# Kernel optimization log

Hardware: AMD Instinct MI355X
Metric: run time of the kernel (lower is better)

The kernel has to match this reference:

```python
import jax, jax.numpy as jnp
import numpy as np

N_NODES = 100000
N_EDGES = 1600000
HIDDEN_DIM = 64
EIGS_DIM = 32


def setup_inputs() -> dict:
    key = jax.random.key(0)
    k1, k2, k3, k4, k5 = jax.random.split(key, 5)
    q = jax.random.normal(k1, (N_NODES, HIDDEN_DIM), dtype=jnp.float32)
    k = jax.random.normal(k2, (N_NODES, HIDDEN_DIM), dtype=jnp.float32)
    v = jax.random.normal(k3, (N_NODES, HIDDEN_DIM), dtype=jnp.float32)
    eigs = jax.random.normal(k4, (N_NODES, EIGS_DIM), dtype=jnp.float32)
    lambda0 = jnp.zeros((1,), dtype=jnp.float32)  # nn.Parameter(torch.zeros(1))
    indices = jax.random.randint(k5, (2, N_EDGES), 0, N_NODES, dtype=jnp.int64)
    return {"q": q, "k": k, "v": v, "eigs": eigs, "lambda0": lambda0,
            "indices": indices}


def reference(q, k, v, eigs, lambda0, indices):
    n = q.shape[0]
    inv_sqrt_dim = 1.0 / jnp.sqrt(jnp.asarray(q.shape[1], dtype=q.dtype))
    i0 = indices[0]  # destination/row node per edge
    i1 = indices[1]  # source/col node per edge

    # per-edge attention logits: gather-dot-product
    x = jnp.sum(q[i0] * k[i1], axis=-1) * inv_sqrt_dim          # [E]
    y = jnp.sum(eigs[i0] * eigs[i1], axis=-1)                   # [E]
    s = x + jnp.exp(lambda0[0]) * y                             # [E]

    # sparse softmax: clamp(exp(s), -5, 5) then segment-normalize by row sum
    e = jnp.clip(jnp.exp(s), -5.0, 5.0)                         # [E]
    denom = jax.ops.segment_sum(e, i0, num_segments=n)          # [N]
    denom = jnp.where(denom == 0.0, 1.0, denom)
    w = e / denom[i0]                                           # [E]

    # spmm: out[r] = sum_{edges with row r} w_e * v[col_e]
    out = jax.ops.segment_sum(w[:, None] * v[i1], i0, num_segments=n)  # [N, D]
    return out
```

## Files before the change

kernel.cpp:

```cpp
#include <hip/hip_runtime.h>


#define HD 64
#define ED 32
#define CAP 64
#define RPP 256
#define PSHIFT 8
#define D1 36
#define NB1 256
#define PCAP 5120
#define SPILL_CAP 131072

__global__ void p1_bin_kernel(const int* __restrict__ idx, int n_edges,
                              int NP, int chunk,
                              int* __restrict__ part, int* __restrict__ gcur,
                              long long* __restrict__ spill,
                              int* __restrict__ spill_cnt,
                              int* __restrict__ flag) {
    extern __shared__ int sm[];
    int* cnt  = sm;
    int* bins = sm + NP;
    int tid = threadIdx.x;

    for (int i = tid; i < NP; i += 256) cnt[i] = 0;
    __syncthreads();

    int e0 = blockIdx.x * chunk;
    int n  = n_edges - e0; if (n > chunk) n = chunk; if (n < 0) n = 0;

    for (int i = tid; i < n; i += 256) {
        int e = e0 + i;
        int r = idx[e];
        int c = idx[n_edges + e];
        int p = r >> PSHIFT;
        int w = ((r & (RPP - 1)) << 17) | c;
        int pos = atomicAdd(&cnt[p], 1);
        if (pos < D1) {
            bins[p * D1 + pos] = w;
        } else {
            int s = atomicAdd(spill_cnt, 1);
            if (s < SPILL_CAP) spill[s] = ((long long)r << 32) | (unsigned)c;
            else *flag = 1;
        }
    }
    __syncthreads();

    for (int p = tid; p < NP; p += 256) {
        int m = cnt[p]; if (m > D1) m = D1;
        if (m > 0) {
            int base = atomicAdd(&gcur[p], m);
            for (int j = 0; j < m; ++j) {
                int slot = base + j;
                int w = bins[p * D1 + j];
                if (slot < PCAP) {
                    part[p * PCAP + slot] = w;
                } else {
                    int r = (p << PSHIFT) | (w >> 17);
                    int c = w & 0x1FFFF;
                    int s = atomicAdd(spill_cnt, 1);
                    if (s < SPILL_CAP) spill[s] = ((long long)r << 32) | (unsigned)c;
                    else *flag = 1;
                }
            }
        }
    }
}

__global__ void p2_bucket_kernel(const int* __restrict__ part,
                                 const int* __restrict__ gcur,
                                 int* __restrict__ count,
                                 int* __restrict__ bucket, int n_nodes) {
    __shared__ int cnt[RPP / 2];
    __shared__ int win[(RPP / 2) * CAP];
    int tid = threadIdx.x;
    if (tid < RPP / 2) cnt[tid] = 0;
    __syncthreads();

    int p    = blockIdx.x >> 1;
    int half = blockIdx.x & 1;
    int n = gcur[p]; if (n > PCAP) n = PCAP;

    for (int i = tid; i < n; i += 256) {
        int w  = part[p * PCAP + i];
        int rl = w >> 17;
        if ((rl >> 7) != half) continue;
        int rh = rl & 127;
        int c  = w & 0x1FFFF;
        int pos = atomicAdd(&cnt[rh], 1);
        if (pos < CAP) win[(rh << 6) + pos] = c;
    }
    __syncthreads();

    int r0 = (p << PSHIFT) + (half << 7);
    int rows = n_nodes - r0;
    if (rows > RPP / 2) rows = RPP / 2;
    if (rows > 0) {
        int nint4 = rows * (CAP / 4);
        int4* dst = (int4*)(bucket + (long long)r0 * CAP);
        const int4* src = (const int4*)win;
        for (int i = tid; i < nint4; i += 256) dst[i] = src[i];
        if (tid < rows) count[r0 + tid] = cnt[tid];
    }
}

__global__ void spill_drain_kernel(const long long* __restrict__ spill,
                                   const int* __restrict__ spill_cnt,
                                   int* __restrict__ count,
                                   int* __restrict__ bucket) {
    int ns = *spill_cnt; if (ns > SPILL_CAP) ns = SPILL_CAP;
    int stride = gridDim.x * blockDim.x;
    for (int t = blockIdx.x * blockDim.x + threadIdx.x; t < ns; t += stride) {
        long long wc = spill[t];
        int r = (int)(wc >> 32);
        int c = (int)(wc & 0xFFFFFFFFLL);
        int pos = atomicAdd(&count[r], 1);
        if (pos < CAP) bucket[(long long)r * CAP + pos] = c;
    }
}

__global__ void repair_zero_kernel(const int* __restrict__ flag,
                                   int* __restrict__ count, int n_nodes) {
    if (*flag == 0) return;
    int t = blockIdx.x * blockDim.x + threadIdx.x;
    if (t < n_nodes) count[t] = 0;
}

__global__ void repair_scatter_kernel(const int* __restrict__ flag,
                                      const int* __restrict__ idx,
                                      int* __restrict__ count,
                                      int* __restrict__ bucket, int n_edges) {
    if (*flag == 0) return;
    int t = blockIdx.x * blockDim.x + threadIdx.x;
    if (t < n_edges) {
        int r = idx[t];
        int c = idx[n_edges + t];
        int p = atomicAdd(&count[r], 1);
        if (p < CAP) bucket[(long long)r * CAP + p] = c;
    }
}

__global__ void bucket_scatter_kernel(const int* __restrict__ idx,
                                      int* __restrict__ count,
                                      int* __restrict__ bucket, int n_edges) {
    int t = blockIdx.x * blockDim.x + threadIdx.x;
    if (t < n_edges) {
        int r = idx[t];
        int c = idx[n_edges + t];
        int p = atomicAdd(&count[r], 1);
        if (p < CAP) bucket[(long long)r * CAP + p] = c;
    }
}

__global__ void row_kernel(const float* __restrict__ q, const float* __restrict__ k,
                           const float* __restrict__ v, const float* __restrict__ eigs,
                           const float* __restrict__ lambda0,
                           const int* __restrict__ counts,
                           const int* __restrict__ col,
                           const int* __restrict__ idx, int n_edges,
                           float* __restrict__ out, int n_nodes) {
    long long tid = (long long)blockIdx.x * blockDim.x + threadIdx.x;
    int r = (int)(tid >> 6);
    if (r >= n_nodes) return;
    int lane = threadIdx.x & 63;
    int sub = lane & 15;
    int grp = lane >> 4;

    int deg = counts[r];
    const float expL = __expf(lambda0[0]);

    if (deg > CAP) {
        float qs = q[(long long)r * HD + lane] * 0.125f;
        float gs = (lane < ED) ? eigs[(long long)r * ED + lane] * expL : 0.f;
        float accs = 0.f, den = 0.f;
        for (int base = 0; base < n_edges; base += 64) {
            int e = base + lane;
            int rr = (e < n_edges) ? idx[e] : -1;
            int cc = (e < n_edges) ? idx[n_edges + e] : 0;
            unsigned long long mm = __ballot(rr == r);
            while (mm) {
                int b = __ffsll(mm) - 1;
                mm &= mm - 1;
                int c = __shfl(cc, b, 64);
                float kb = k[(long long)c * HD + lane];
                float gb = (lane < ED) ? eigs[(long long)c * ED + lane] : 0.f;
                float s = qs * kb + gs * gb;
                #pragma unroll
                for (int off = 32; off > 0; off >>= 1) s += __shfl_xor(s, off, 64);
                float e1 = fminf(__expf(s), 5.0f);
                den += e1;
                accs += e1 * v[(long long)c * HD + lane];
            }
        }
        float inv = (den == 0.f) ? 1.f : __frcp_rn(den);
        out[(long long)r * HD + lane] = accs * inv;
        return;
    }

    long long start = (long long)r * CAP;

    float4 qa = *(const float4*)(q    + (long long)r * HD + sub * 4);
    float2 ga = *(const float2*)(eigs + (long long)r * ED + sub * 2);
    qa.x *= 0.125f; qa.y *= 0.125f; qa.z *= 0.125f; qa.w *= 0.125f;
    ga.x *= expL;   ga.y *= expL;

    float4 acc = make_float4(0.f, 0.f, 0.f, 0.f);
    float den = 0.f;

    for (int base = 0; base < deg; base += 64) {
        int m = deg - base; if (m > 64) m = 64;
        int cl = (lane < m) ? col[start + base + lane] : 0;
        for (int j = 0; j < m; j += 16) {
            int c1 = __shfl(cl, j + grp,      64);
            int c2 = __shfl(cl, j + 4 + grp,  64);
            int c3 = __shfl(cl, j + 8 + grp,  64);
            int c4 = __shfl(cl, j + 12 + grp, 64);
            float4 kb1 = *(const float4*)(k    + (long long)c1 * HD + sub * 4);
            float2 gb1 = *(const float2*)(eigs + (long long)c1 * ED + sub * 2);
            float4 vv1 = *(const float4*)(v    + (long long)c1 * HD + sub * 4);
            float4 kb2 = *(const float4*)(k    + (long long)c2 * HD + sub * 4);
            float2 gb2 = *(const float2*)(eigs + (long long)c2 * ED + sub * 2);
            float4 vv2 = *(const float4*)(v    + (long long)c2 * HD + sub * 4);
            float4 kb3 = *(const float4*)(k    + (long long)c3 * HD + sub * 4);
            float2 gb3 = *(const float2*)(eigs + (long long)c3 * ED + sub * 2);
            float4 vv3 = *(const float4*)(v    + (long long)c3 * HD + sub * 4);
            float4 kb4 = *(const float4*)(k    + (long long)c4 * HD + sub * 4);
            float2 gb4 = *(const float2*)(eigs + (long long)c4 * ED + sub * 2);
            float4 vv4 = *(const float4*)(v    + (long long)c4 * HD + sub * 4);

            float s1 = qa.x*kb1.x + qa.y*kb1.y + qa.z*kb1.z + qa.w*kb1.w
                     + ga.x*gb1.x + ga.y*gb1.y;
            float s2 = qa.x*kb2.x + qa.y*kb2.y + qa.z*kb2.z + qa.w*kb2.w
                     + ga.x*gb2.x + ga.y*gb2.y;
            float s3 = qa.x*kb3.x + qa.y*kb3.y + qa.z*kb3.z + qa.w*kb3.w
                     + ga.x*gb3.x + ga.y*gb3.y;
            float s4 = qa.x*kb4.x + qa.y*kb4.y + qa.z*kb4.z + qa.w*kb4.w
                     + ga.x*gb4.x + ga.y*gb4.y;
            #pragma unroll
            for (int off = 8; off > 0; off >>= 1) {
                s1 += __shfl_xor(s1, off, 64);
                s2 += __shfl_xor(s2, off, 64);
                s3 += __shfl_xor(s3, off, 64);
                s4 += __shfl_xor(s4, off, 64);
            }
            float e1 = fminf(__expf(s1), 5.0f);
            float e2 = fminf(__expf(s2), 5.0f);
            float e3 = fminf(__expf(s3), 5.0f);
            float e4 = fminf(__expf(s4), 5.0f);

            if (j + grp < m) {
                den += e1;
                acc.x += e1 * vv1.x; acc.y += e1 * vv1.y;
                acc.z += e1 * vv1.z; acc.w += e1 * vv1.w;
            }
            if (j + 4 + grp < m) {
                den += e2;
                acc.x += e2 * vv2.x; acc.y += e2 * vv2.y;
                acc.z += e2 * vv2.z; acc.w += e2 * vv2.w;
            }
            if (j + 8 + grp < m) {
                den += e3;
                acc.x += e3 * vv3.x; acc.y += e3 * vv3.y;
                acc.z += e3 * vv3.z; acc.w += e3 * vv3.w;
            }
            if (j + 12 + grp < m) {
                den += e4;
                acc.x += e4 * vv4.x; acc.y += e4 * vv4.y;
                acc.z += e4 * vv4.z; acc.w += e4 * vv4.w;
            }
        }
    }

    #pragma unroll
    for (int off = 16; off < 64; off <<= 1) {
        acc.x += __shfl_xor(acc.x, off, 64);
        acc.y += __shfl_xor(acc.y, off, 64);
        acc.z += __shfl_xor(acc.z, off, 64);
        acc.w += __shfl_xor(acc.w, off, 64);
        den   += __shfl_xor(den,   off, 64);
    }

    if (grp == 0) {
        float inv = (den == 0.0f) ? 1.0f : __frcp_rn(den);
        float4 o = make_float4(acc.x * inv, acc.y * inv, acc.z * inv, acc.w * inv);
        *(float4*)(out + (long long)r * HD + sub * 4) = o;
    }
}

__global__ void edge_fused_kernel(const float* __restrict__ q,
                                  const float* __restrict__ k,
                                  const float* __restrict__ v,
                                  const float* __restrict__ eigs,
                                  const float* __restrict__ lambda0,
                                  const int* __restrict__ idx,
                                  float* __restrict__ denom,
                                  float* __restrict__ out, int n_edges) {
    long long gid = (long long)blockIdx.x * blockDim.x + threadIdx.x;
    int lane = threadIdx.x & 63;
    int edge = (int)(gid >> 4);
    int sub  = (int)(gid & 15);
    int valid = (edge < n_edges);
    int ec = valid ? edge : (n_edges - 1);
    int i0 = idx[ec];
    int i1 = idx[n_edges + ec];
    const float expL = __expf(lambda0[0]);
    float4 qa = *(const float4*)(q + (long long)i0 * HD + sub * 4);
    float4 kb = *(const float4*)(k + (long long)i1 * HD + sub * 4);
    float c = (qa.x*kb.x + qa.y*kb.y + qa.z*kb.z + qa.w*kb.w) * 0.125f;
    float2 ea = *(const float2*)(eigs + (long long)i0 * ED + sub * 2);
    float2 eb = *(const float2*)(eigs + (long long)i1 * ED + sub * 2);
    c += expL * (ea.x * eb.x + ea.y * eb.y);
    #pragma unroll
    for (int off = 8; off > 0; off >>= 1) c += __shfl_xor(c, off, 64);
    float e = fminf(__expf(c), 5.0f);
    if (valid && sub == 0) atomicAdd(&denom[i0], e);
    #pragma unroll
    for (int j = 0; j < 4; ++j) {
        float ej = __shfl(e,     j * 16, 64);
        int   r  = __shfl(i0,    j * 16, 64);
        int   s  = __shfl(i1,    j * 16, 64);
        int   vj = __shfl(valid, j * 16, 64);
        if (vj) {
            float vv = v[(long long)s * HD + lane];
            atomicAdd(&out[(long long)r * HD + lane], ej * vv);
        }
    }
}

__global__ void normalize_kernel(float* __restrict__ out,
                                 const float* __restrict__ denom, int n_nodes) {
    int t = blockIdx.x * blockDim.x + threadIdx.x;
    int total = n_nodes * (HD / 4);
    if (t >= total) return;
    int row = t >> 4;
    float d = denom[row];
    float inv = (d == 0.0f) ? 1.0f : __frcp_rn(d);
    float4* o4 = (float4*)out;
    float4 x = o4[t];
    x.x *= inv; x.y *= inv; x.z *= inv; x.w *= inv;
    o4[t] = x;
}

extern "C" void kernel_launch(void* const* d_in, const int* in_sizes, int n_in,
                              void* d_out, int out_size, void* d_ws, size_t ws_size,
                              hipStream_t stream) {
    const float* q       = (const float*)d_in[0];
    const float* k       = (const float*)d_in[1];
    const float* v       = (const float*)d_in[2];
    const float* eigs    = (const float*)d_in[3];
    const float* lambda0 = (const float*)d_in[4];
    const int*   idx     = (const int*)d_in[5];

    const int n_edges = in_sizes[5] / 2;
    const int n_nodes = in_sizes[0] / HD;

    const int NP = (n_nodes + RPP - 1) / RPP;
    const int eb = (n_edges + 255) / 256;
    long long rthreads = (long long)n_nodes * 64;
    const int rb = (int)((rthreads + 255) / 256);

    size_t need1 = ((size_t)n_nodes + (size_t)n_nodes * CAP
                    + (size_t)NP * PCAP + NP + 2) * sizeof(int)
                 + (size_t)SPILL_CAP * sizeof(long long);
    size_t need2 = ((size_t)n_nodes + (size_t)n_nodes * CAP) * sizeof(int);

    if (ws_size >= need1) {
        int* count     = (int*)d_ws;
        int* bucket    = count + n_nodes;
        int* part      = bucket + (size_t)n_nodes * CAP;
        int* gcur      = part + (size_t)NP * PCAP;
        int* spill_cnt = gcur + NP;
        int* flag      = spill_cnt + 1;
        long long* spill = (long long*)(flag + 1);

        hipMemsetAsync(gcur, 0, (size_t)(NP + 2) * sizeof(int), stream);

        int chunk = (n_edges + NB1 - 1) / NB1;
        size_t smbytes = (size_t)NP * (1 + D1) * sizeof(int);
        p1_bin_kernel<<<NB1, 256, smbytes, stream>>>(idx, n_edges, NP, chunk,
                                                     part, gcur, spill,
                                                     spill_cnt, flag);
        p2_bucket_kernel<<<2 * NP, 256, 0, stream>>>(part, gcur, count, bucket,
                                                     n_nodes);
        spill_drain_kernel<<<256, 256, 0, stream>>>(spill, spill_cnt, count,
                                                    bucket);
        repair_zero_kernel<<<(n_nodes + 255) / 256, 256, 0, stream>>>(flag, count,
                                                                      n_nodes);
        repair_scatter_kernel<<<eb, 256, 0, stream>>>(flag, idx, count, bucket,
                                                      n_edges);
        row_kernel<<<rb, 256, 0, stream>>>(q, k, v, eigs, lambda0, count, bucket,
                                           idx, n_edges, (float*)d_out, n_nodes);
    } else if (ws_size >= need2) {
        int* count  = (int*)d_ws;
        int* bucket = count + n_nodes;
        hipMemsetAsync(count, 0, (size_t)n_nodes * sizeof(int), stream);
        bucket_scatter_kernel<<<eb, 256, 0, stream>>>(idx, count, bucket, n_edges);
        row_kernel<<<rb, 256, 0, stream>>>(q, k, v, eigs, lambda0, count, bucket,
                                           idx, n_edges, (float*)d_out, n_nodes);
    } else {
        float* denom = (float*)d_ws;
        hipMemsetAsync(denom, 0, (size_t)n_nodes * sizeof(float), stream);
        hipMemsetAsync(d_out, 0, (size_t)out_size * sizeof(float), stream);
        long long threads = (long long)n_edges * 16;
        int grid = (int)((threads + 255) / 256);
        edge_fused_kernel<<<grid, 256, 0, stream>>>(q, k, v, eigs, lambda0, idx,
                                                    denom, (float*)d_out, n_edges);
        int n4 = n_nodes * (HD / 4);
        normalize_kernel<<<(n4 + 255) / 256, 256, 0, stream>>>((float*)d_out,
                                                               denom, n_nodes);
    }
}
```

Baseline: 297.5 us.

## Gather K, V and eigs from fp16 copies in the row kernel

Adds a conversion pass that writes half-precision copies of k, v and eigs into the workspace. A new row kernel gathers from these copies, which halves the random-gather traffic per edge, and falls back to fp32 for overflow rows. The binning flush is also reworked to use one wave per partition instead of a serial per-thread loop. The fallback row kernel's unroll is reduced to two edges per step. In exchange it adds three conversion launches over all nodes and fp16 rounding error in the logits and outputs.

```diff
diff --git a/kernel.cpp b/kernel.cpp
--- a/kernel.cpp
+++ b/kernel.cpp
@@ -1,4 +1,5 @@
 #include <hip/hip_runtime.h>
+#include <hip/hip_fp16.h>
 
 
 #define HD 64
@@ -10,6 +11,21 @@
 #define NB1 256
 #define PCAP 5120
 #define SPILL_CAP 131072
+
+struct h4 { __half2 a, b; };
+
+__global__ void cvt16_kernel(const float* __restrict__ src,
+                             __half* __restrict__ dst, long long n4) {
+    long long t = (long long)blockIdx.x * blockDim.x + threadIdx.x;
+    long long stride = (long long)gridDim.x * blockDim.x;
+    for (; t < n4; t += stride) {
+        float4 f = ((const float4*)src)[t];
+        h4 h;
+        h.a = __floats2half2_rn(f.x, f.y);
+        h.b = __floats2half2_rn(f.z, f.w);
+        ((h4*)dst)[t] = h;
+    }
+}
 
 __global__ void p1_bin_kernel(const int* __restrict__ idx, int n_edges,
                               int NP, int chunk,
@@ -45,22 +61,25 @@
     }
     __syncthreads();
 
-    for (int p = tid; p < NP; p += 256) {
+    int wave = tid >> 6;
+    int lane = tid & 63;
+    for (int p = wave; p < NP; p += 4) {
         int m = cnt[p]; if (m > D1) m = D1;
-        if (m > 0) {
-            int base = atomicAdd(&gcur[p], m);
-            for (int j = 0; j < m; ++j) {
-                int slot = base + j;
-                int w = bins[p * D1 + j];
-                if (slot < PCAP) {
-                    part[p * PCAP + slot] = w;
-                } else {
-                    int r = (p << PSHIFT) | (w >> 17);
-                    int c = w & 0x1FFFF;
-                    int s = atomicAdd(spill_cnt, 1);
-                    if (s < SPILL_CAP) spill[s] = ((long long)r << 32) | (unsigned)c;
-                    else *flag = 1;
-                }
+        if (m == 0) continue;
+        int base = 0;
+        if (lane == 0) base = atomicAdd(&gcur[p], m);
+        base = __shfl(base, 0, 64);
+        if (lane < m) {
+            int slot = base + lane;
+            int w = bins[p * D1 + lane];
+            if (slot < PCAP) {
+                part[p * PCAP + slot] = w;
+            } else {
+                int r = (p << PSHIFT) | (w >> 17);
+                int c = w & 0x1FFFF;
+                int s = atomicAdd(spill_cnt, 1);
+                if (s < SPILL_CAP) spill[s] = ((long long)r << 32) | (unsigned)c;
+                else *flag = 1;
             }
         }
     }
@@ -148,6 +167,150 @@
         int c = idx[n_edges + t];
         int p = atomicAdd(&count[r], 1);
         if (p < CAP) bucket[(long long)r * CAP + p] = c;
+    }
+}
+
+__global__ void row16_kernel(const float* __restrict__ q,
+                             const __half* __restrict__ k16,
+                             const __half* __restrict__ v16,
+                             const float* __restrict__ eigs,
+                             const __half* __restrict__ e16,
+                             const float* __restrict__ lambda0,
+                             const int* __restrict__ counts,
+                             const int* __restrict__ col,
+                             const float* __restrict__ kf,
+                             const float* __restrict__ vf,
+                             const int* __restrict__ idx, int n_edges,
+                             float* __restrict__ out, int n_nodes) {
+    long long tid = (long long)blockIdx.x * blockDim.x + threadIdx.x;
+    int r = (int)(tid >> 6);
+    if (r >= n_nodes) return;
+    int lane = threadIdx.x & 63;
+    int sub = lane & 15;
+    int grp = lane >> 4;
+
+    int deg = counts[r];
+    const float expL = __expf(lambda0[0]);
+
+    if (deg > CAP) {
+        float qs = q[(long long)r * HD + lane] * 0.125f;
+        float gs = (lane < ED) ? eigs[(long long)r * ED + lane] * expL : 0.f;
+        float accs = 0.f, den = 0.f;
+        for (int base = 0; base < n_edges; base += 64) {
+            int e = base + lane;
+            int rr = (e < n_edges) ? idx[e] : -1;
+            int cc = (e < n_edges) ? idx[n_edges + e] : 0;
+            unsigned long long mm = __ballot(rr == r);
+            while (mm) {
+                int b = __ffsll(mm) - 1;
+                mm &= mm - 1;
+                int c = __shfl(cc, b, 64);
+                float kb = kf[(long long)c * HD + lane];
+                float gb = (lane < ED) ? eigs[(long long)c * ED + lane] : 0.f;
+                float s = qs * kb + gs * gb;
+                #pragma unroll
+                for (int off = 32; off > 0; off >>= 1) s += __shfl_xor(s, off, 64);
+                float e1 = fminf(__expf(s), 5.0f);
+                den += e1;
+                accs += e1 * vf[(long long)c * HD + lane];
+            }
+        }
+        float inv = (den == 0.f) ? 1.f : __frcp_rn(den);
+        out[(long long)r * HD + lane] = accs * inv;
+        return;
+    }
+
+    long long start = (long long)r * CAP;
+
+    float4 qa = *(const float4*)(q    + (long long)r * HD + sub * 4);
+    float2 ga = *(const float2*)(eigs + (long long)r * ED + sub * 2);
+    qa.x *= 0.125f; qa.y *= 0.125f; qa.z *= 0.125f; qa.w *= 0.125f;
+    ga.x *= expL;   ga.y *= expL;
+
+    float4 acc = make_float4(0.f, 0.f, 0.f, 0.f);
+    float den = 0.f;
+
+    for (int base = 0; base < deg; base += 64) {
+        int m = deg - base; if (m > 64) m = 64;
+        int cl = (lane < m) ? col[start + base + lane] : 0;
+        for (int j = 0; j < m; j += 16) {
+            int c1 = __shfl(cl, j + grp,      64);
+            int c2 = __shfl(cl, j + 4 + grp,  64);
+            int c3 = __shfl(cl, j + 8 + grp,  64);
+            int c4 = __shfl(cl, j + 12 + grp, 64);
+            h4 kb1 = *(const h4*)(k16 + (long long)c1 * HD + sub * 4);
+            __half2 gh1 = *(const __half2*)(e16 + (long long)c1 * ED + sub * 2);
+            h4 vv1 = *(const h4*)(v16 + (long long)c1 * HD + sub * 4);
+            h4 kb2 = *(const h4*)(k16 + (long long)c2 * HD + sub * 4);
+            __half2 gh2 = *(const __half2*)(e16 + (long long)c2 * ED + sub * 2);
+            h4 vv2 = *(const h4*)(v16 + (long long)c2 * HD + sub * 4);
+            h4 kb3 = *(const h4*)(k16 + (long long)c3 * HD + sub * 4);
+            __half2 gh3 = *(const __half2*)(e16 + (long long)c3 * ED + sub * 2);
+            h4 vv3 = *(const h4*)(v16 + (long long)c3 * HD + sub * 4);
+            h4 kb4 = *(const h4*)(k16 + (long long)c4 * HD + sub * 4);
+            __half2 gh4 = *(const __half2*)(e16 + (long long)c4 * ED + sub * 2);
+            h4 vv4 = *(const h4*)(v16 + (long long)c4 * HD + sub * 4);
+
+            float s1 = qa.x*__low2float(kb1.a) + qa.y*__high2float(kb1.a)
+                     + qa.z*__low2float(kb1.b) + qa.w*__high2float(kb1.b)
+                     + ga.x*__low2float(gh1)   + ga.y*__high2float(gh1);
+            float s2 = qa.x*__low2float(kb2.a) + qa.y*__high2float(kb2.a)
+                     + qa.z*__low2float(kb2.b) + qa.w*__high2float(kb2.b)
+                     + ga.x*__low2float(gh2)   + ga.y*__high2float(gh2);
+            float s3 = qa.x*__low2float(kb3.a) + qa.y*__high2float(kb3.a)
+                     + qa.z*__low2float(kb3.b) + qa.w*__high2float(kb3.b)
+                     + ga.x*__low2float(gh3)   + ga.y*__high2float(gh3);
+            float s4 = qa.x*__low2float(kb4.a) + qa.y*__high2float(kb4.a)
+                     + qa.z*__low2float(kb4.b) + qa.w*__high2float(kb4.b)
+                     + ga.x*__low2float(gh4)   + ga.y*__high2float(gh4);
+            #pragma unroll
+            for (int off = 8; off > 0; off >>= 1) {
+                s1 += __shfl_xor(s1, off, 64);
+                s2 += __shfl_xor(s2, off, 64);
+                s3 += __shfl_xor(s3, off, 64);
+                s4 += __shfl_xor(s4, off, 64);
+            }
+            float e1 = fminf(__expf(s1), 5.0f);
+            float e2 = fminf(__expf(s2), 5.0f);
+            float e3 = fminf(__expf(s3), 5.0f);
+            float e4 = fminf(__expf(s4), 5.0f);
+
+            if (j + grp < m) {
+                den += e1;
+                acc.x += e1 * __low2float(vv1.a); acc.y += e1 * __high2float(vv1.a);
+                acc.z += e1 * __low2float(vv1.b); acc.w += e1 * __high2float(vv1.b);
+            }
+            if (j + 4 + grp < m) {
+                den += e2;
+                acc.x += e2 * __low2float(vv2.a); acc.y += e2 * __high2float(vv2.a);
+                acc.z += e2 * __low2float(vv2.b); acc.w += e2 * __high2float(vv2.b);
+            }
+            if (j + 8 + grp < m) {
+                den += e3;
+                acc.x += e3 * __low2float(vv3.a); acc.y += e3 * __high2float(vv3.a);
+                acc.z += e3 * __low2float(vv3.b); acc.w += e3 * __high2float(vv3.b);
+            }
+            if (j + 12 + grp < m) {
+                den += e4;
+                acc.x += e4 * __low2float(vv4.a); acc.y += e4 * __high2float(vv4.a);
+                acc.z += e4 * __low2float(vv4.b); acc.w += e4 * __high2float(vv4.b);
+            }
+        }
+    }
+
+    #pragma unroll
+    for (int off = 16; off < 64; off <<= 1) {
+        acc.x += __shfl_xor(acc.x, off, 64);
+        acc.y += __shfl_xor(acc.y, off, 64);
+        acc.z += __shfl_xor(acc.z, off, 64);
+        acc.w += __shfl_xor(acc.w, off, 64);
+        den   += __shfl_xor(den,   off, 64);
+    }
+
+    if (grp == 0) {
+        float inv = (den == 0.0f) ? 1.0f : __frcp_rn(den);
+        float4 o = make_float4(acc.x * inv, acc.y * inv, acc.z * inv, acc.w * inv);
+        *(float4*)(out + (long long)r * HD + sub * 4) = o;
     }
 }
 
@@ -209,43 +372,27 @@
     for (int base = 0; base < deg; base += 64) {
         int m = deg - base; if (m > 64) m = 64;
         int cl = (lane < m) ? col[start + base + lane] : 0;
-        for (int j = 0; j < m; j += 16) {
-            int c1 = __shfl(cl, j + grp,      64);
-            int c2 = __shfl(cl, j + 4 + grp,  64);
-            int c3 = __shfl(cl, j + 8 + grp,  64);
-            int c4 = __shfl(cl, j + 12 + grp, 64);
+        for (int j = 0; j < m; j += 8) {
+            int c1 = __shfl(cl, j + grp,     64);
+            int c2 = __shfl(cl, j + 4 + grp, 64);
             float4 kb1 = *(const float4*)(k    + (long long)c1 * HD + sub * 4);
             float2 gb1 = *(const float2*)(eigs + (long long)c1 * ED + sub * 2);
             float4 vv1 = *(const float4*)(v    + (long long)c1 * HD + sub * 4);
             float4 kb2 = *(const float4*)(k    + (long long)c2 * HD + sub * 4);
             float2 gb2 = *(const float2*)(eigs + (long long)c2 * ED + sub * 2);
             float4 vv2 = *(const float4*)(v    + (long long)c2 * HD + sub * 4);
-            float4 kb3 = *(const float4*)(k    + (long long)c3 * HD + sub * 4);
-            float2 gb3 = *(const float2*)(eigs + (long long)c3 * ED + sub * 2);
-            float4 vv3 = *(const float4*)(v    + (long long)c3 * HD + sub * 4);
-            float4 kb4 = *(const float4*)(k    + (long long)c4 * HD + sub * 4);
-            float2 gb4 = *(const float2*)(eigs + (long long)c4 * ED + sub * 2);
-            float4 vv4 = *(const float4*)(v    + (long long)c4 * HD + sub * 4);
 
             float s1 = qa.x*kb1.x + qa.y*kb1.y + qa.z*kb1.z + qa.w*kb1.w
                      + ga.x*gb1.x + ga.y*gb1.y;
             float s2 = qa.x*kb2.x + qa.y*kb2.y + qa.z*kb2.z + qa.w*kb2.w
                      + ga.x*gb2.x + ga.y*gb2.y;
-            float s3 = qa.x*kb3.x + qa.y*kb3.y + qa.z*kb3.z + qa.w*kb3.w
-                     + ga.x*gb3.x + ga.y*gb3.y;
-            float s4 = qa.x*kb4.x + qa.y*kb4.y + qa.z*kb4.z + qa.w*kb4.w
-                     + ga.x*gb4.x + ga.y*gb4.y;
             #pragma unroll
             for (int off = 8; off > 0; off >>= 1) {
                 s1 += __shfl_xor(s1, off, 64);
                 s2 += __shfl_xor(s2, off, 64);
-                s3 += __shfl_xor(s3, off, 64);
-                s4 += __shfl_xor(s4, off, 64);
             }
             float e1 = fminf(__expf(s1), 5.0f);
             float e2 = fminf(__expf(s2), 5.0f);
-            float e3 = fminf(__expf(s3), 5.0f);
-            float e4 = fminf(__expf(s4), 5.0f);
 
             if (j + grp < m) {
                 den += e1;
@@ -256,16 +403,6 @@
                 den += e2;
                 acc.x += e2 * vv2.x; acc.y += e2 * vv2.y;
                 acc.z += e2 * vv2.z; acc.w += e2 * vv2.w;
-            }
-            if (j + 8 + grp < m) {
-                den += e3;
-                acc.x += e3 * vv3.x; acc.y += e3 * vv3.y;
-                acc.z += e3 * vv3.z; acc.w += e3 * vv3.w;
-            }
-            if (j + 12 + grp < m) {
-                den += e4;
-                acc.x += e4 * vv4.x; acc.y += e4 * vv4.y;
-                acc.z += e4 * vv4.z; acc.w += e4 * vv4.w;
             }
         }
     }
@@ -361,9 +498,44 @@
     size_t need1 = ((size_t)n_nodes + (size_t)n_nodes * CAP
                     + (size_t)NP * PCAP + NP + 2) * sizeof(int)
                  + (size_t)SPILL_CAP * sizeof(long long);
+    size_t need16 = need1 + (size_t)n_nodes * (HD + HD + ED) * sizeof(__half);
     size_t need2 = ((size_t)n_nodes + (size_t)n_nodes * CAP) * sizeof(int);
 
-    if (ws_size >= need1) {
+    if (ws_size >= need16) {
+        int* count     = (int*)d_ws;
+        int* bucket    = count + n_nodes;
+        int* part      = bucket + (size_t)n_nodes * CAP;
+        int* gcur      = part + (size_t)NP * PCAP;
+        int* spill_cnt = gcur + NP;
+        int* flag      = spill_cnt + 1;
+        long long* spill = (long long*)(flag + 1);
+        __half* k16 = (__half*)(spill + SPILL_CAP);
+        __half* v16 = k16 + (size_t)n_nodes * HD;
+        __half* e16 = v16 + (size_t)n_nodes * HD;
+
+        hipMemsetAsync(gcur, 0, (size_t)(NP + 2) * sizeof(int), stream);
+
+        cvt16_kernel<<<1024, 256, 0, stream>>>(k, k16, (long long)n_nodes * HD / 4);
+        cvt16_kernel<<<1024, 256, 0, stream>>>(v, v16, (long long)n_nodes * HD / 4);
+        cvt16_kernel<<<1024, 256, 0, stream>>>(eigs, e16, (long long)n_nodes * ED / 4);
+
+        int chunk = (n_edges + NB1 - 1) / NB1;
+        size_t smbytes = (size_t)NP * (1 + D1) * sizeof(int);
+        p1_bin_kernel<<<NB1, 256, smbytes, stream>>>(idx, n_edges, NP, chunk,
+                                                     part, gcur, spill,
+                                                     spill_cnt, flag);
+        p2_bucket_kernel<<<2 * NP, 256, 0, stream>>>(part, gcur, count, bucket,
+                                                     n_nodes);
+        spill_drain_kernel<<<256, 256, 0, stream>>>(spill, spill_cnt, count,
+                                                    bucket);
+        repair_zero_kernel<<<(n_nodes + 255) / 256, 256, 0, stream>>>(flag, count,
+                                                                      n_nodes);
+        repair_scatter_kernel<<<eb, 256, 0, stream>>>(flag, idx, count, bucket,
+                                                      n_edges);
+        row16_kernel<<<rb, 256, 0, stream>>>(q, k16, v16, eigs, e16, lambda0,
+                                             count, bucket, k, v, idx, n_edges,
+                                             (float*)d_out, n_nodes);
+    } else if (ws_size >= need1) {
         int* count     = (int*)d_ws;
         int* bucket    = count + n_nodes;
         int* part      = bucket + (size_t)n_nodes * CAP;
```

New measurement: 594.7 us. 99.9% more time.
